# Performance work log

Hardware: AMD Instinct MI355X
Metric: run time of the kernel (lower is better)

Reference implementation:

```python
import jax, jax.numpy as jnp
import numpy as np

B, S, H = 16, 1024, 256
NH = 4
DH = H // NH


def setup_inputs() -> dict:
    key = jax.random.key(0)
    ks = jax.random.split(key, 12)
    w = lambda i, shape: jax.random.normal(ks[i], shape, dtype=jnp.float32) * 0.02
    return {
        "step_sequence": jax.random.normal(ks[0], (B, S, H), dtype=jnp.float32),
        "final_outcomes": jax.random.normal(ks[1], (B,), dtype=jnp.float32),
        "step_mask": jnp.ones((B, S), dtype=jnp.bool_),
        # MultiheadAttention q/k projections (only attn weights are used)
        "Wq": w(2, (H, H)), "bq": jnp.zeros((H,), jnp.float32),
        "Wk": w(3, (H, H)), "bk": jnp.zeros((H,), jnp.float32),
        # causal_mask_predictor: Linear(H,H//2)-ReLU-Linear(H//2,1)-Sigmoid
        "Wm1": w(4, (H, H // 2)), "bm1": jnp.zeros((H // 2,), jnp.float32),
        "Wm2": w(5, (H // 2, 1)), "bm2": jnp.zeros((1,), jnp.float32),
        # intervention_generator: Linear(H,H)-ReLU-Linear(H,H)-Tanh
        "Wi1": w(6, (H, H)), "bi1": jnp.zeros((H,), jnp.float32),
        "Wi2": w(7, (H, H)), "bi2": jnp.zeros((H,), jnp.float32),
        # credit_estimator: Linear(H,H//2)-ReLU-Linear(H//2,1)
        "We1": w(8, (H, H // 2)), "be1": jnp.zeros((H // 2,), jnp.float32),
        "We2": w(9, (H // 2, 1)), "be2": jnp.zeros((1,), jnp.float32),
    }


def _forward(x, final_outcomes, step_mask, Wq, bq, Wk, bk, Wm1, bm1, Wm2, bm2,
             Wi1, bi1, Wi2, bi2, We1, be1, We2, be2):
    # --- CausalAttentionModule ---
    q = (x @ Wq + bq).reshape(B, S, NH, DH).transpose(0, 2, 1, 3)  # [B,NH,S,DH]
    k = (x @ Wk + bk).reshape(B, S, NH, DH).transpose(0, 2, 1, 3)
    scores = jnp.einsum('bhqd,bhkd->bhqk', q, k) / jnp.sqrt(jnp.float32(DH))
    scores = jnp.where(step_mask[:, None, None, :], scores, -jnp.inf)  # key_padding_mask
    attn = jax.nn.softmax(scores, axis=-1).mean(axis=1)  # head-averaged [B,S,S]
    strengths = jax.nn.sigmoid(jax.nn.relu(x @ Wm1 + bm1) @ Wm2 + bm2)[..., 0]  # [B,S]
    aw_mean = attn.mean(axis=1)  # mean over query dim -> [B,S]
    cm = aw_mean[:, None, :] * strengths[:, :, None]  # [B,S,S]
    cm = cm * jnp.tril(jnp.ones((S, S), dtype=x.dtype))[None]
    # --- interventional credit (vectorized over the B x S python loop) ---
    colmean = cm.mean(axis=1)  # mean_i cm[b,i,j] -> [B,S]
    base = (x * colmean[..., None]).mean(axis=1)  # [B,H] baseline weighted-mean feature
    # intervention changes only row t: delta = 0.1*tanh-MLP(x_t)
    delta = 0.1 * jnp.tanh(jax.nn.relu(x @ Wi1 + bi1) @ Wi2 + bi2)  # [B,S,H]
    feats = base[:, None, :] + delta * colmean[..., None] / S  # [B,S,H]
    outcomes = (jax.nn.relu(feats @ We1 + be1) @ We2 + be2)[..., 0]  # [B,S]
    credit = jnp.where(step_mask, final_outcomes[:, None] - outcomes, 0.0)
    return credit, cm


def reference(step_sequence, final_outcomes, step_mask, Wq, bq, Wk, bk,
              Wm1, bm1, Wm2, bm2, Wi1, bi1, Wi2, bi2, We1, be1, We2, be2):
    return _forward(step_sequence, final_outcomes, step_mask, Wq, bq, Wk, bk,
                    Wm1, bm1, Wm2, bm2, Wi1, bi1, Wi2, bi2, We1, be1, We2, be2)
```

## Files before the change

### kernel.cpp

```cpp
#include <hip/hip_runtime.h>
#include <hip/hip_bf16.h>
#include <math.h>

#define B 16
#define S 1024
#define H 256
#define NH 4
#define DH 64
#define BS (B*S)
#define XSTR 264

typedef short short8 __attribute__((ext_vector_type(8)));
typedef float f32x16 __attribute__((ext_vector_type(16)));

__device__ __forceinline__ unsigned short to_bf16(float v) {
  __hip_bfloat16 h = __float2bfloat16(v);
  return *(unsigned short*)&h;
}

__global__ __launch_bounds__(256) void k_convert_x(
    const float* __restrict__ x, unsigned short* __restrict__ xb)
{
  int i = blockIdx.x * 256 + threadIdx.x;
  float4 v = ((const float4*)x)[i];
  uint2 pk;
  pk.x = (unsigned int)to_bf16(v.x) | ((unsigned int)to_bf16(v.y) << 16);
  pk.y = (unsigned int)to_bf16(v.z) | ((unsigned int)to_bf16(v.w) << 16);
  ((uint2*)xb)[i] = pk;
}

__global__ __launch_bounds__(256) void k_convert_w(
    const float* __restrict__ Wq, const float* __restrict__ Wk,
    const float* __restrict__ Wm1, const float* __restrict__ Wi1,
    const float* __restrict__ Wi2, const float* __restrict__ We1,
    unsigned short* __restrict__ WqT, unsigned short* __restrict__ WkT,
    unsigned short* __restrict__ Wm1T, unsigned short* __restrict__ Wi1T,
    unsigned short* __restrict__ Wi2T, unsigned short* __restrict__ We1T)
{
  const float* src; unsigned short* dst; int N;
  switch (blockIdx.y) {
    case 0: src = Wq;  dst = WqT;  N = 256; break;
    case 1: src = Wk;  dst = WkT;  N = 256; break;
    case 2: src = Wm1; dst = Wm1T; N = 128; break;
    case 3: src = Wi1; dst = Wi1T; N = 256; break;
    case 4: src = Wi2; dst = Wi2T; N = 256; break;
    default: src = We1; dst = We1T; N = 128; break;
  }
  int ntiles = N >> 5;
  int tile = blockIdx.x;
  if (tile >= 8 * ntiles) return;
  int kt = tile / ntiles, nt = tile % ntiles;
  __shared__ float tl[32][33];
  int t = threadIdx.x, r = t >> 5, c = t & 31;
  #pragma unroll
  for (int i = 0; i < 4; ++i)
    tl[r + i*8][c] = src[(kt*32 + r + i*8)*N + nt*32 + c];
  __syncthreads();
  #pragma unroll
  for (int i = 0; i < 4; ++i)
    dst[(nt*32 + r + i*8)*256 + kt*32 + c] = to_bf16(tl[c][r + i*8]);
}

__global__ __launch_bounds__(256) void k_qkproj_mfma(
    const unsigned short* __restrict__ xb,
    const unsigned short* __restrict__ WqT, const unsigned short* __restrict__ WkT,
    const float* __restrict__ bq, const float* __restrict__ bk,
    unsigned short* __restrict__ qbuf, unsigned short* __restrict__ kbuf)
{
  __shared__ unsigned short xs[32*XSTR];
  int t = threadIdx.x, wave = t >> 6, lane = t & 63;
  int l5 = lane & 31, h5 = lane >> 5;
  int gx = blockIdx.x, gy = blockIdx.y;
  int r0 = gx * 32;
  const unsigned short* WT = gy ? WkT : WqT;
  const float* biasp = gy ? bk : bq;
  float scale = gy ? 1.f : 0.125f;
  {
    const uint4* s4 = (const uint4*)(xb + (size_t)r0 * H);
    #pragma unroll
    for (int it = 0; it < 4; ++it) {
      int u = it*256 + t, r = u >> 5, c = u & 31;
      *(uint4*)&xs[r*XSTR + c*8] = s4[u];
    }
  }
  __syncthreads();
  f32x16 acc0, acc1;
  #pragma unroll
  for (int r = 0; r < 16; ++r) { acc0[r] = 0.f; acc1[r] = 0.f; }
  int n0 = wave*64 + l5;
  #pragma unroll 8
  for (int kc = 0; kc < 16; ++kc) {
    short8 a = *(const short8*)&xs[l5*XSTR + kc*16 + h5*8];
    short8 b0 = *(const short8*)&WT[(size_t)n0*256 + kc*16 + h5*8];
    short8 b1 = *(const short8*)&WT[(size_t)(n0+32)*256 + kc*16 + h5*8];
    acc0 = __builtin_amdgcn_mfma_f32_32x32x16_bf16(a, b0, acc0, 0, 0, 0);
    acc1 = __builtin_amdgcn_mfma_f32_32x32x16_bf16(a, b1, acc1, 0, 0, 0);
  }
  __syncthreads();
  float bi0 = biasp[n0], bi1v = biasp[n0 + 32];
  #pragma unroll
  for (int r = 0; r < 16; ++r) {
    int row = (r & 3) + 8*(r >> 2) + 4*h5;
    xs[row*XSTR + n0]      = to_bf16((acc0[r] + bi0) * scale);
    xs[row*XSTR + n0 + 32] = to_bf16((acc1[r] + bi1v) * scale);
  }
  __syncthreads();
  unsigned short* outp = gy ? kbuf : qbuf;
  #pragma unroll
  for (int it = 0; it < 4; ++it) {
    int u = it*256 + t, r = u >> 5, c8 = u & 31;
    int mg = r0 + r, bb = mg >> 10, s = mg & 1023;
    int hh = c8 >> 3, dd = (c8 & 7) * 8;
    *(uint4*)&outp[(size_t)(((bb*NH + hh)*S + s)*DH + dd)] = *(uint4*)&xs[r*XSTR + c8*8];
  }
}

__global__ __launch_bounds__(256) void k_strengths_mfma(
    const unsigned short* __restrict__ xb, const unsigned short* __restrict__ Wm1T,
    const float* __restrict__ bm1, const float* __restrict__ Wm2, const float* __restrict__ bm2,
    float* __restrict__ strengths)
{
  __shared__ unsigned short xs[32*XSTR];
  __shared__ float red[4][32];
  int t = threadIdx.x, wave = t >> 6, lane = t & 63;
  int l5 = lane & 31, h5 = lane >> 5;
  int r0 = blockIdx.x * 32;
  {
    const uint4* s4 = (const uint4*)(xb + (size_t)r0 * H);
    #pragma unroll
    for (int it = 0; it < 4; ++it) {
      int u = it*256 + t, r = u >> 5, c = u & 31;
      *(uint4*)&xs[r*XSTR + c*8] = s4[u];
    }
  }
  __syncthreads();
  f32x16 acc;
  #pragma unroll
  for (int r = 0; r < 16; ++r) acc[r] = 0.f;
  int n = wave*32 + l5;
  #pragma unroll 8
  for (int kc = 0; kc < 16; ++kc) {
    short8 a = *(const short8*)&xs[l5*XSTR + kc*16 + h5*8];
    short8 b = *(const short8*)&Wm1T[(size_t)n*256 + kc*16 + h5*8];
    acc = __builtin_amdgcn_mfma_f32_32x32x16_bf16(a, b, acc, 0, 0, 0);
  }
  float bi = bm1[n], w2 = Wm2[n];
  #pragma unroll
  for (int r = 0; r < 16; ++r) {
    float v = fmaxf(acc[r] + bi, 0.f) * w2;
    #pragma unroll
    for (int off = 1; off <= 16; off <<= 1) v += __shfl_xor(v, off);
    if (l5 == 0) red[wave][(r & 3) + 8*(r >> 2) + 4*h5] = v;
  }
  __syncthreads();
  if (t < 32) {
    float s = red[0][t] + red[1][t] + red[2][t] + red[3][t] + bm2[0];
    strengths[r0 + t] = 1.f / (1.f + __expf(-s));
  }
}

#define KSTRIDE 72
__global__ __launch_bounds__(256) void k_attn_mfma(
    const unsigned short* __restrict__ qbuf, const unsigned short* __restrict__ kbuf,
    float* __restrict__ aw_sum)
{
  __shared__ unsigned short Ks[128*KSTRIDE];
  __shared__ unsigned short Qs[64*KSTRIDE];
  int t = threadIdx.x;
  int wave = t >> 6, lane = t & 63;
  int l5 = lane & 31, h5 = lane >> 5;
  int i0 = blockIdx.x * 64;
  int h = blockIdx.y, b = blockIdx.z;
  const unsigned short* qg = qbuf + (size_t)((b*NH + h)*S + i0) * DH;
  const unsigned short* kg = kbuf + (size_t)((b*NH + h)*S) * DH;
  {
    const uint4* src = (const uint4*)qg;
    #pragma unroll
    for (int it = 0; it < 2; ++it) {
      int u = it*256 + t, r = u >> 3, c = u & 7;
      *(uint4*)&Qs[r*KSTRIDE + c*8] = src[u];
    }
  }
  __syncthreads();
  short8 af[2][4];
  #pragma unroll
  for (int rt = 0; rt < 2; ++rt)
    #pragma unroll
    for (int kc = 0; kc < 4; ++kc)
      af[rt][kc] = *(const short8*)&Qs[(rt*32 + l5)*KSTRIDE + kc*16 + h5*8];
  float lacc[2][16];
  #pragma unroll
  for (int rt = 0; rt < 2; ++rt)
    #pragma unroll
    for (int r = 0; r < 16; ++r) lacc[rt][r] = 0.f;
  const uint4* ksrc = (const uint4*)kg;
  for (int pass = 0; pass < 2; ++pass) {
    for (int kt = 0; kt < 8; ++kt) {
      __syncthreads();
      #pragma unroll
      for (int it = 0; it < 4; ++it) {
        int u = it*256 + t, r = u >> 3, c = u & 7;
        *(uint4*)&Ks[r*KSTRIDE + c*8] = ksrc[kt*1024 + u];
      }
      __syncthreads();
      short8 bfr[4];
      #pragma unroll
      for (int kc = 0; kc < 4; ++kc)
        bfr[kc] = *(const short8*)&Ks[(wave*32 + l5)*KSTRIDE + kc*16 + h5*8];
      float csum = 0.f;
      #pragma unroll
      for (int rt = 0; rt < 2; ++rt) {
        f32x16 acc;
        #pragma unroll
        for (int r = 0; r < 16; ++r) acc[r] = 0.f;
        #pragma unroll
        for (int kc = 0; kc < 4; ++kc)
          acc = __builtin_amdgcn_mfma_f32_32x32x16_bf16(af[rt][kc], bfr[kc], acc, 0, 0, 0);
        if (pass == 0) {
          #pragma unroll
          for (int r = 0; r < 16; ++r) lacc[rt][r] += __expf(acc[r]);
        } else {
          #pragma unroll
          for (int r = 0; r < 16; ++r) csum += __expf(acc[r]) * lacc[rt][r];
        }
      }
      if (pass == 1) {
        csum += __shfl_xor(csum, 32);
        if (lane < 32)
          atomicAdd(&aw_sum[b*S + kt*128 + wave*32 + lane], csum);
      }
    }
    if (pass == 0) {
      #pragma unroll
      for (int rt = 0; rt < 2; ++rt)
        #pragma unroll
        for (int r = 0; r < 16; ++r) {
          float v = lacc[rt][r];
          #pragma unroll
          for (int off = 1; off <= 16; off <<= 1) v += __shfl_xor(v, off);
          lacc[rt][r] = 1.f / v;
        }
    }
  }
}

__global__ __launch_bounds__(256) void k_colmean(
    const float* __restrict__ strengths, const float* __restrict__ aw_sum,
    float* __restrict__ aw_mean, float* __restrict__ colmean)
{
  __shared__ float st[1024];
  int t = threadIdx.x, b = blockIdx.x;
  #pragma unroll
  for (int e = 0; e < 4; ++e) st[t + e*256] = strengths[b*S + t + e*256];
  __syncthreads();
  for (int off = 1; off < 1024; off <<= 1) {
    float tmp[4];
    #pragma unroll
    for (int e = 0; e < 4; ++e) {
      int j = t + e*256;
      tmp[e] = (j + off < 1024) ? st[j + off] : 0.f;
    }
    __syncthreads();
    #pragma unroll
    for (int e = 0; e < 4; ++e) st[t + e*256] += tmp[e];
    __syncthreads();
  }
  #pragma unroll
  for (int e = 0; e < 4; ++e) {
    int j = t + e*256;
    float am = aw_sum[b*S + j] * (1.f / (NH * (float)S));
    aw_mean[b*S + j] = am;
    colmean[b*S + j] = am * st[j] * (1.f / (float)S);
  }
}

__global__ __launch_bounds__(256) void k_cm(
    const float* __restrict__ aw_mean, const float* __restrict__ strengths,
    float* __restrict__ cm_out)
{
  int t = threadIdx.x;
  int row = blockIdx.x;
  int b = row >> 10, i = row & 1023;
  float sti = strengths[row];
  float4 v = ((const float4*)(aw_mean + b*S))[t];
  int j0 = t * 4;
  float4 o;
  o.x = (j0 + 0 <= i) ? v.x * sti : 0.f;
  o.y = (j0 + 1 <= i) ? v.y * sti : 0.f;
  o.z = (j0 + 2 <= i) ? v.z * sti : 0.f;
  o.w = (j0 + 3 <= i) ? v.w * sti : 0.f;
  ((float4*)cm_out)[(size_t)row*(S/4) + t] = o;
}

__global__ __launch_bounds__(256) void k_base(
    const float* __restrict__ x, const float* __restrict__ colmean,
    float* __restrict__ base)
{
  int t = threadIdx.x;
  int chunk = blockIdx.x, b = blockIdx.y;
  float acc = 0.f;
  int t0 = chunk * 32;
  for (int tt = 0; tt < 32; ++tt) {
    int srow = t0 + tt;
    acc += x[(size_t)(b*S + srow)*H + t] * colmean[b*S + srow];
  }
  atomicAdd(&base[b*H + t], acc * (1.f / (float)S));
}

__global__ __launch_bounds__(256) void k_credit_mfma(
    const unsigned short* __restrict__ xb, const float* __restrict__ base,
    const float* __restrict__ colmean,
    const unsigned short* __restrict__ Wi1T, const float* __restrict__ bi1,
    const unsigned short* __restrict__ Wi2T, const float* __restrict__ bi2,
    const unsigned short* __restrict__ We1T, const float* __restrict__ be1,
    const float* __restrict__ We2, const float* __restrict__ be2,
    const float* __restrict__ final_outcomes, float* __restrict__ credit_out)
{
  __shared__ unsigned short xs[32*XSTR];
  __shared__ unsigned short hs[32*XSTR];
  __shared__ float cmv_s[32];
  __shared__ float red[4][32];
  int t = threadIdx.x, wave = t >> 6, lane = t & 63;
  int l5 = lane & 31, h5 = lane >> 5;
  int r0 = blockIdx.x * 32;
  int b = r0 >> 10;
  {
    const uint4* s4 = (const uint4*)(xb + (size_t)r0 * H);
    #pragma unroll
    for (int it = 0; it < 4; ++it) {
      int u = it*256 + t, r = u >> 5, c = u & 31;
      *(uint4*)&xs[r*XSTR + c*8] = s4[u];
    }
  }
  if (t < 32) cmv_s[t] = colmean[r0 + t];
  __syncthreads();

  int n0 = wave*64 + l5;
  {
    f32x16 acc0, acc1;
    #pragma unroll
    for (int r = 0; r < 16; ++r) { acc0[r] = 0.f; acc1[r] = 0.f; }
    #pragma unroll 8
    for (int kc = 0; kc < 16; ++kc) {
      short8 a = *(const short8*)&xs[l5*XSTR + kc*16 + h5*8];
      short8 b0 = *(const short8*)&Wi1T[(size_t)n0*256 + kc*16 + h5*8];
      short8 b1 = *(const short8*)&Wi1T[(size_t)(n0+32)*256 + kc*16 + h5*8];
      acc0 = __builtin_amdgcn_mfma_f32_32x32x16_bf16(a, b0, acc0, 0, 0, 0);
      acc1 = __builtin_amdgcn_mfma_f32_32x32x16_bf16(a, b1, acc1, 0, 0, 0);
    }
    float bi0 = bi1[n0], biv1 = bi1[n0 + 32];
    #pragma unroll
    for (int r = 0; r < 16; ++r) {
      int row = (r & 3) + 8*(r >> 2) + 4*h5;
      hs[row*XSTR + n0]      = to_bf16(fmaxf(acc0[r] + bi0, 0.f));
      hs[row*XSTR + n0 + 32] = to_bf16(fmaxf(acc1[r] + biv1, 0.f));
    }
  }
  __syncthreads();
  {
    f32x16 acc0, acc1;
    #pragma unroll
    for (int r = 0; r < 16; ++r) { acc0[r] = 0.f; acc1[r] = 0.f; }
    #pragma unroll 8
    for (int kc = 0; kc < 16; ++kc) {
      short8 a = *(const short8*)&hs[l5*XSTR + kc*16 + h5*8];
      short8 b0 = *(const short8*)&Wi2T[(size_t)n0*256 + kc*16 + h5*8];
      short8 b1 = *(const short8*)&Wi2T[(size_t)(n0+32)*256 + kc*16 + h5*8];
      acc0 = __builtin_amdgcn_mfma_f32_32x32x16_bf16(a, b0, acc0, 0, 0, 0);
      acc1 = __builtin_amdgcn_mfma_f32_32x32x16_bf16(a, b1, acc1, 0, 0, 0);
    }
    float bi0 = bi2[n0], biv1 = bi2[n0 + 32];
    float bb0 = base[b*H + n0], bb1 = base[b*H + n0 + 32];
    __syncthreads();
    #pragma unroll
    for (int r = 0; r < 16; ++r) {
      int row = (r & 3) + 8*(r >> 2) + 4*h5;
      float cmv = cmv_s[row] * (0.1f / (float)S);
      float e0 = __expf(2.f*(acc0[r] + bi0));
      float e1 = __expf(2.f*(acc1[r] + biv1));
      float th0 = (e0 - 1.f) / (e0 + 1.f);
      float th1 = (e1 - 1.f) / (e1 + 1.f);
      xs[row*XSTR + n0]      = to_bf16(bb0 + th0 * cmv);
      xs[row*XSTR + n0 + 32] = to_bf16(bb1 + th1 * cmv);
    }
  }
  __syncthreads();
  {
    f32x16 acc;
    #pragma unroll
    for (int r = 0; r < 16; ++r) acc[r] = 0.f;
    int n = wave*32 + l5;
    #pragma unroll 8
    for (int kc = 0; kc < 16; ++kc) {
      short8 a = *(const short8*)&xs[l5*XSTR + kc*16 + h5*8];
      short8 bfrag = *(const short8*)&We1T[(size_t)n*256 + kc*16 + h5*8];
      acc = __builtin_amdgcn_mfma_f32_32x32x16_bf16(a, bfrag, acc, 0, 0, 0);
    }
    float bev = be1[n], w2 = We2[n];
    #pragma unroll
    for (int r = 0; r < 16; ++r) {
      float v = fmaxf(acc[r] + bev, 0.f) * w2;
      #pragma unroll
      for (int off = 1; off <= 16; off <<= 1) v += __shfl_xor(v, off);
      if (l5 == 0) red[wave][(r & 3) + 8*(r >> 2) + 4*h5] = v;
    }
  }
  __syncthreads();
  if (t < 32) {
    float s = red[0][t] + red[1][t] + red[2][t] + red[3][t] + be2[0];
    credit_out[r0 + t] = final_outcomes[b] - s;
  }
}

extern "C" void kernel_launch(void* const* d_in, const int* in_sizes, int n_in,
                              void* d_out, int out_size, void* d_ws, size_t ws_size,
                              hipStream_t stream) {
  (void)in_sizes; (void)n_in; (void)out_size; (void)ws_size;
  const float* x   = (const float*)d_in[0];
  const float* fin = (const float*)d_in[1];
  const float* Wq  = (const float*)d_in[3];  const float* bq  = (const float*)d_in[4];
  const float* Wk  = (const float*)d_in[5];  const float* bk  = (const float*)d_in[6];
  const float* Wm1 = (const float*)d_in[7];  const float* bm1 = (const float*)d_in[8];
  const float* Wm2 = (const float*)d_in[9];  const float* bm2 = (const float*)d_in[10];
  const float* Wi1 = (const float*)d_in[11]; const float* bi1 = (const float*)d_in[12];
  const float* Wi2 = (const float*)d_in[13]; const float* bi2 = (const float*)d_in[14];
  const float* We1 = (const float*)d_in[15]; const float* be1 = (const float*)d_in[16];
  const float* We2 = (const float*)d_in[17]; const float* be2 = (const float*)d_in[18];

  unsigned short* us = (unsigned short*)d_ws;
  unsigned short* xb   = us;
  unsigned short* qb   = xb + (size_t)BS*H;
  unsigned short* kb   = qb + (size_t)B*NH*S*DH;
  unsigned short* WqT  = kb + (size_t)B*NH*S*DH;
  unsigned short* WkT  = WqT + 65536;
  unsigned short* Wi1T = WkT + 65536;
  unsigned short* Wi2T = Wi1T + 65536;
  unsigned short* Wm1T = Wi2T + 65536;
  unsigned short* We1T = Wm1T + 32768;
  float* fs = (float*)(We1T + 32768);
  float* aw_sum    = fs;
  float* strengths = aw_sum + BS;
  float* aw_mean   = strengths + BS;
  float* colmean   = aw_mean + BS;
  float* base      = colmean + BS;

  float* credit_out = (float*)d_out;
  float* cm_out     = credit_out + BS;

  hipMemsetAsync(aw_sum, 0, BS*sizeof(float), stream);
  hipMemsetAsync(base, 0, B*H*sizeof(float), stream);

  k_convert_x     <<<BS*H/1024, 256, 0, stream>>>(x, xb);
  k_convert_w     <<<dim3(64, 6), 256, 0, stream>>>(Wq, Wk, Wm1, Wi1, Wi2, We1,
                                                    WqT, WkT, Wm1T, Wi1T, Wi2T, We1T);
  k_qkproj_mfma   <<<dim3(BS/32, 2), 256, 0, stream>>>(xb, WqT, WkT, bq, bk, qb, kb);
  k_strengths_mfma<<<BS/32, 256, 0, stream>>>(xb, Wm1T, bm1, Wm2, bm2, strengths);
  k_attn_mfma     <<<dim3(S/64, NH, B), 256, 0, stream>>>(qb, kb, aw_sum);
  k_colmean       <<<B, 256, 0, stream>>>(strengths, aw_sum, aw_mean, colmean);
  k_cm            <<<BS, 256, 0, stream>>>(aw_mean, strengths, cm_out);
  k_base          <<<dim3(32, B), 256, 0, stream>>>(x, colmean, base);
  k_credit_mfma   <<<BS/32, 256, 0, stream>>>(xb, base, colmean, Wi1T, bi1, Wi2T, bi2,
                                              We1T, be1, We2, be2, fin, credit_out);
}
```

Measured before the change: 238.1 us.

## Fuse x conversion into consumers, single-pass attention softmax, drop atomics

Removes the separate x-to-bf16 conversion kernel and converts fp32 x on the fly inside the projection, strengths and credit kernels. Q and K projections are computed in one block sharing the x tile, and the Q scale folds in log2(e) so attention can use hardware exp2. Attention is restructured into a single pass over keys that caches bf16-packed probabilities in registers instead of recomputing scores. Atomics and memsets are replaced by per-tile partial buffers that later kernels sum. This trades heavy register pressure and extra partial-sum reads for fewer launches, less recomputation and no atomic contention.

```diff
diff --git a/kernel.cpp b/kernel.cpp
--- a/kernel.cpp
+++ b/kernel.cpp
@@ -9,6 +9,7 @@
 #define DH 64
 #define BS (B*S)
 #define XSTR 264
+#define L2E 1.4426950408889634f
 
 typedef short short8 __attribute__((ext_vector_type(8)));
 typedef float f32x16 __attribute__((ext_vector_type(16)));
@@ -17,16 +18,11 @@
   __hip_bfloat16 h = __float2bfloat16(v);
   return *(unsigned short*)&h;
 }
-
-__global__ __launch_bounds__(256) void k_convert_x(
-    const float* __restrict__ x, unsigned short* __restrict__ xb)
-{
-  int i = blockIdx.x * 256 + threadIdx.x;
-  float4 v = ((const float4*)x)[i];
-  uint2 pk;
-  pk.x = (unsigned int)to_bf16(v.x) | ((unsigned int)to_bf16(v.y) << 16);
-  pk.y = (unsigned int)to_bf16(v.z) | ((unsigned int)to_bf16(v.w) << 16);
-  ((uint2*)xb)[i] = pk;
+__device__ __forceinline__ unsigned int pack_bf16x2(float a, float b) {
+  return (unsigned int)to_bf16(a) | ((unsigned int)to_bf16(b) << 16);
+}
+__device__ __forceinline__ float exp2_hw(float v) {
+  return __builtin_amdgcn_exp2f(v);
 }
 
 __global__ __launch_bounds__(256) void k_convert_w(
@@ -62,7 +58,7 @@
 }
 
 __global__ __launch_bounds__(256) void k_qkproj_mfma(
-    const unsigned short* __restrict__ xb,
+    const float* __restrict__ x,
     const unsigned short* __restrict__ WqT, const unsigned short* __restrict__ WkT,
     const float* __restrict__ bq, const float* __restrict__ bk,
     unsigned short* __restrict__ qbuf, unsigned short* __restrict__ kbuf)
@@ -70,53 +66,75 @@
   __shared__ unsigned short xs[32*XSTR];
   int t = threadIdx.x, wave = t >> 6, lane = t & 63;
   int l5 = lane & 31, h5 = lane >> 5;
-  int gx = blockIdx.x, gy = blockIdx.y;
-  int r0 = gx * 32;
-  const unsigned short* WT = gy ? WkT : WqT;
-  const float* biasp = gy ? bk : bq;
-  float scale = gy ? 1.f : 0.125f;
-  {
-    const uint4* s4 = (const uint4*)(xb + (size_t)r0 * H);
-    #pragma unroll
-    for (int it = 0; it < 4; ++it) {
-      int u = it*256 + t, r = u >> 5, c = u & 31;
-      *(uint4*)&xs[r*XSTR + c*8] = s4[u];
-    }
-  }
-  __syncthreads();
-  f32x16 acc0, acc1;
-  #pragma unroll
-  for (int r = 0; r < 16; ++r) { acc0[r] = 0.f; acc1[r] = 0.f; }
+  int r0 = blockIdx.x * 32;
+  {
+    const float4* xg = (const float4*)(x + (size_t)r0*H);
+    #pragma unroll
+    for (int it = 0; it < 8; ++it) {
+      int u = it*256 + t, r = u >> 6, c4 = u & 63;
+      float4 v = xg[u];
+      uint2 pk; pk.x = pack_bf16x2(v.x, v.y); pk.y = pack_bf16x2(v.z, v.w);
+      *(uint2*)&xs[r*XSTR + c4*4] = pk;
+    }
+  }
+  __syncthreads();
   int n0 = wave*64 + l5;
+  f32x16 aq0, aq1, ak0, ak1;
+  #pragma unroll
+  for (int r = 0; r < 16; ++r) { aq0[r]=0.f; aq1[r]=0.f; ak0[r]=0.f; ak1[r]=0.f; }
   #pragma unroll 8
   for (int kc = 0; kc < 16; ++kc) {
-    short8 a = *(const short8*)&xs[l5*XSTR + kc*16 + h5*8];
-    short8 b0 = *(const short8*)&WT[(size_t)n0*256 + kc*16 + h5*8];
-    short8 b1 = *(const short8*)&WT[(size_t)(n0+32)*256 + kc*16 + h5*8];
-    acc0 = __builtin_amdgcn_mfma_f32_32x32x16_bf16(a, b0, acc0, 0, 0, 0);
-    acc1 = __builtin_amdgcn_mfma_f32_32x32x16_bf16(a, b1, acc1, 0, 0, 0);
-  }
-  __syncthreads();
-  float bi0 = biasp[n0], bi1v = biasp[n0 + 32];
-  #pragma unroll
-  for (int r = 0; r < 16; ++r) {
-    int row = (r & 3) + 8*(r >> 2) + 4*h5;
-    xs[row*XSTR + n0]      = to_bf16((acc0[r] + bi0) * scale);
-    xs[row*XSTR + n0 + 32] = to_bf16((acc1[r] + bi1v) * scale);
-  }
-  __syncthreads();
-  unsigned short* outp = gy ? kbuf : qbuf;
+    short8 a  = *(const short8*)&xs[l5*XSTR + kc*16 + h5*8];
+    short8 q0 = *(const short8*)&WqT[(size_t)n0*256 + kc*16 + h5*8];
+    short8 q1 = *(const short8*)&WqT[(size_t)(n0+32)*256 + kc*16 + h5*8];
+    short8 k0 = *(const short8*)&WkT[(size_t)n0*256 + kc*16 + h5*8];
+    short8 k1 = *(const short8*)&WkT[(size_t)(n0+32)*256 + kc*16 + h5*8];
+    aq0 = __builtin_amdgcn_mfma_f32_32x32x16_bf16(a, q0, aq0, 0, 0, 0);
+    aq1 = __builtin_amdgcn_mfma_f32_32x32x16_bf16(a, q1, aq1, 0, 0, 0);
+    ak0 = __builtin_amdgcn_mfma_f32_32x32x16_bf16(a, k0, ak0, 0, 0, 0);
+    ak1 = __builtin_amdgcn_mfma_f32_32x32x16_bf16(a, k1, ak1, 0, 0, 0);
+  }
+  const float qsc = 0.125f * L2E;
+  __syncthreads();
+  {
+    float b0 = bq[n0], b1 = bq[n0+32];
+    #pragma unroll
+    for (int r = 0; r < 16; ++r) {
+      int row = (r & 3) + 8*(r >> 2) + 4*h5;
+      xs[row*XSTR + n0]      = to_bf16((aq0[r] + b0) * qsc);
+      xs[row*XSTR + n0 + 32] = to_bf16((aq1[r] + b1) * qsc);
+    }
+  }
+  __syncthreads();
   #pragma unroll
   for (int it = 0; it < 4; ++it) {
     int u = it*256 + t, r = u >> 5, c8 = u & 31;
     int mg = r0 + r, bb = mg >> 10, s = mg & 1023;
     int hh = c8 >> 3, dd = (c8 & 7) * 8;
-    *(uint4*)&outp[(size_t)(((bb*NH + hh)*S + s)*DH + dd)] = *(uint4*)&xs[r*XSTR + c8*8];
+    *(uint4*)&qbuf[(size_t)(((bb*NH + hh)*S + s)*DH + dd)] = *(uint4*)&xs[r*XSTR + c8*8];
+  }
+  __syncthreads();
+  {
+    float b0 = bk[n0], b1 = bk[n0+32];
+    #pragma unroll
+    for (int r = 0; r < 16; ++r) {
+      int row = (r & 3) + 8*(r >> 2) + 4*h5;
+      xs[row*XSTR + n0]      = to_bf16(ak0[r] + b0);
+      xs[row*XSTR + n0 + 32] = to_bf16(ak1[r] + b1);
+    }
+  }
+  __syncthreads();
+  #pragma unroll
+  for (int it = 0; it < 4; ++it) {
+    int u = it*256 + t, r = u >> 5, c8 = u & 31;
+    int mg = r0 + r, bb = mg >> 10, s = mg & 1023;
+    int hh = c8 >> 3, dd = (c8 & 7) * 8;
+    *(uint4*)&kbuf[(size_t)(((bb*NH + hh)*S + s)*DH + dd)] = *(uint4*)&xs[r*XSTR + c8*8];
   }
 }
 
 __global__ __launch_bounds__(256) void k_strengths_mfma(
-    const unsigned short* __restrict__ xb, const unsigned short* __restrict__ Wm1T,
+    const float* __restrict__ x, const unsigned short* __restrict__ Wm1T,
     const float* __restrict__ bm1, const float* __restrict__ Wm2, const float* __restrict__ bm2,
     float* __restrict__ strengths)
 {
@@ -126,11 +144,13 @@
   int l5 = lane & 31, h5 = lane >> 5;
   int r0 = blockIdx.x * 32;
   {
-    const uint4* s4 = (const uint4*)(xb + (size_t)r0 * H);
-    #pragma unroll
-    for (int it = 0; it < 4; ++it) {
-      int u = it*256 + t, r = u >> 5, c = u & 31;
-      *(uint4*)&xs[r*XSTR + c*8] = s4[u];
+    const float4* xg = (const float4*)(x + (size_t)r0*H);
+    #pragma unroll
+    for (int it = 0; it < 8; ++it) {
+      int u = it*256 + t, r = u >> 6, c4 = u & 63;
+      float4 v = xg[u];
+      uint2 pk; pk.x = pack_bf16x2(v.x, v.y); pk.y = pack_bf16x2(v.z, v.w);
+      *(uint2*)&xs[r*XSTR + c4*4] = pk;
     }
   }
   __syncthreads();
@@ -159,93 +179,101 @@
   }
 }
 
-#define KSTRIDE 72
 __global__ __launch_bounds__(256) void k_attn_mfma(
     const unsigned short* __restrict__ qbuf, const unsigned short* __restrict__ kbuf,
-    float* __restrict__ aw_sum)
-{
-  __shared__ unsigned short Ks[128*KSTRIDE];
-  __shared__ unsigned short Qs[64*KSTRIDE];
-  int t = threadIdx.x;
-  int wave = t >> 6, lane = t & 63;
+    float* __restrict__ aw_part)
+{
+  __shared__ float part[4][64];
+  int t = threadIdx.x, wave = t >> 6, lane = t & 63;
   int l5 = lane & 31, h5 = lane >> 5;
-  int i0 = blockIdx.x * 64;
+  int qt = blockIdx.x, i0 = qt * 64;
   int h = blockIdx.y, b = blockIdx.z;
   const unsigned short* qg = qbuf + (size_t)((b*NH + h)*S + i0) * DH;
   const unsigned short* kg = kbuf + (size_t)((b*NH + h)*S) * DH;
-  {
-    const uint4* src = (const uint4*)qg;
-    #pragma unroll
-    for (int it = 0; it < 2; ++it) {
-      int u = it*256 + t, r = u >> 3, c = u & 7;
-      *(uint4*)&Qs[r*KSTRIDE + c*8] = src[u];
-    }
-  }
-  __syncthreads();
+
   short8 af[2][4];
   #pragma unroll
   for (int rt = 0; rt < 2; ++rt)
     #pragma unroll
     for (int kc = 0; kc < 4; ++kc)
-      af[rt][kc] = *(const short8*)&Qs[(rt*32 + l5)*KSTRIDE + kc*16 + h5*8];
+      af[rt][kc] = *(const short8*)(qg + (rt*32 + l5)*DH + kc*16 + h5*8);
+
   float lacc[2][16];
   #pragma unroll
   for (int rt = 0; rt < 2; ++rt)
     #pragma unroll
     for (int r = 0; r < 16; ++r) lacc[rt][r] = 0.f;
-  const uint4* ksrc = (const uint4*)kg;
-  for (int pass = 0; pass < 2; ++pass) {
-    for (int kt = 0; kt < 8; ++kt) {
-      __syncthreads();
+
+  unsigned int pp[8][2][8];
+  #pragma unroll
+  for (int kt = 0; kt < 8; ++kt) {
+    short8 bfr[4];
+    #pragma unroll
+    for (int kc = 0; kc < 4; ++kc)
+      bfr[kc] = *(const short8*)(kg + (size_t)(kt*128 + wave*32 + l5)*DH + kc*16 + h5*8);
+    f32x16 a0, a1;
+    #pragma unroll
+    for (int r = 0; r < 16; ++r) { a0[r] = 0.f; a1[r] = 0.f; }
+    #pragma unroll
+    for (int kc = 0; kc < 4; ++kc) {
+      a0 = __builtin_amdgcn_mfma_f32_32x32x16_bf16(af[0][kc], bfr[kc], a0, 0, 0, 0);
+      a1 = __builtin_amdgcn_mfma_f32_32x32x16_bf16(af[1][kc], bfr[kc], a1, 0, 0, 0);
+    }
+    #pragma unroll
+    for (int r2 = 0; r2 < 8; ++r2) {
+      float p0 = exp2_hw(a0[2*r2]), p1 = exp2_hw(a0[2*r2+1]);
+      lacc[0][2*r2] += p0; lacc[0][2*r2+1] += p1;
+      pp[kt][0][r2] = pack_bf16x2(p0, p1);
+      float q0 = exp2_hw(a1[2*r2]), q1 = exp2_hw(a1[2*r2+1]);
+      lacc[1][2*r2] += q0; lacc[1][2*r2+1] += q1;
+      pp[kt][1][r2] = pack_bf16x2(q0, q1);
+    }
+  }
+  #pragma unroll
+  for (int rt = 0; rt < 2; ++rt)
+    #pragma unroll
+    for (int r = 0; r < 16; ++r) {
+      float v = lacc[rt][r];
       #pragma unroll
-      for (int it = 0; it < 4; ++it) {
-        int u = it*256 + t, r = u >> 3, c = u & 7;
-        *(uint4*)&Ks[r*KSTRIDE + c*8] = ksrc[kt*1024 + u];
+      for (int off = 1; off <= 16; off <<= 1) v += __shfl_xor(v, off);
+      lacc[rt][r] = v;
+    }
+  if (l5 == 0) {
+    #pragma unroll
+    for (int rt = 0; rt < 2; ++rt)
+      #pragma unroll
+      for (int r = 0; r < 16; ++r)
+        part[wave][rt*32 + (r & 3) + 8*(r >> 2) + 4*h5] = lacc[rt][r];
+  }
+  __syncthreads();
+  float linv[2][16];
+  #pragma unroll
+  for (int rt = 0; rt < 2; ++rt)
+    #pragma unroll
+    for (int r = 0; r < 16; ++r) {
+      int row = rt*32 + (r & 3) + 8*(r >> 2) + 4*h5;
+      linv[rt][r] = 1.f / (part[0][row] + part[1][row] + part[2][row] + part[3][row]);
+    }
+  #pragma unroll
+  for (int kt = 0; kt < 8; ++kt) {
+    float csum = 0.f;
+    #pragma unroll
+    for (int rt = 0; rt < 2; ++rt)
+      #pragma unroll
+      for (int r2 = 0; r2 < 8; ++r2) {
+        unsigned int u = pp[kt][rt][r2];
+        float p0 = __uint_as_float(u << 16);
+        float p1 = __uint_as_float(u & 0xffff0000u);
+        csum += p0 * linv[rt][2*r2] + p1 * linv[rt][2*r2+1];
       }
-      __syncthreads();
-      short8 bfr[4];
-      #pragma unroll
-      for (int kc = 0; kc < 4; ++kc)
-        bfr[kc] = *(const short8*)&Ks[(wave*32 + l5)*KSTRIDE + kc*16 + h5*8];
-      float csum = 0.f;
-      #pragma unroll
-      for (int rt = 0; rt < 2; ++rt) {
-        f32x16 acc;
-        #pragma unroll
-        for (int r = 0; r < 16; ++r) acc[r] = 0.f;
-        #pragma unroll
-        for (int kc = 0; kc < 4; ++kc)
-          acc = __builtin_amdgcn_mfma_f32_32x32x16_bf16(af[rt][kc], bfr[kc], acc, 0, 0, 0);
-        if (pass == 0) {
-          #pragma unroll
-          for (int r = 0; r < 16; ++r) lacc[rt][r] += __expf(acc[r]);
-        } else {
-          #pragma unroll
-          for (int r = 0; r < 16; ++r) csum += __expf(acc[r]) * lacc[rt][r];
-        }
-      }
-      if (pass == 1) {
-        csum += __shfl_xor(csum, 32);
-        if (lane < 32)
-          atomicAdd(&aw_sum[b*S + kt*128 + wave*32 + lane], csum);
-      }
-    }
-    if (pass == 0) {
-      #pragma unroll
-      for (int rt = 0; rt < 2; ++rt)
-        #pragma unroll
-        for (int r = 0; r < 16; ++r) {
-          float v = lacc[rt][r];
-          #pragma unroll
-          for (int off = 1; off <= 16; off <<= 1) v += __shfl_xor(v, off);
-          lacc[rt][r] = 1.f / v;
-        }
-    }
+    csum += __shfl_xor(csum, 32);
+    if (lane < 32)
+      aw_part[(size_t)qt*BS + b*S + kt*128 + wave*32 + lane] = csum;
   }
 }
 
 __global__ __launch_bounds__(256) void k_colmean(
-    const float* __restrict__ strengths, const float* __restrict__ aw_sum,
+    const float* __restrict__ strengths, const float* __restrict__ aw_part,
     float* __restrict__ aw_mean, float* __restrict__ colmean)
 {
   __shared__ float st[1024];
@@ -268,7 +296,10 @@
   #pragma unroll
   for (int e = 0; e < 4; ++e) {
     int j = t + e*256;
-    float am = aw_sum[b*S + j] * (1.f / (NH * (float)S));
+    float s = 0.f;
+    #pragma unroll
+    for (int qt = 0; qt < 16; ++qt) s += aw_part[(size_t)qt*BS + b*S + j];
+    float am = s * (1.f / (NH * (float)S));
     aw_mean[b*S + j] = am;
     colmean[b*S + j] = am * st[j] * (1.f / (float)S);
   }
@@ -294,7 +325,7 @@
 
 __global__ __launch_bounds__(256) void k_base(
     const float* __restrict__ x, const float* __restrict__ colmean,
-    float* __restrict__ base)
+    float* __restrict__ base_part)
 {
   int t = threadIdx.x;
   int chunk = blockIdx.x, b = blockIdx.y;
@@ -304,11 +335,11 @@
     int srow = t0 + tt;
     acc += x[(size_t)(b*S + srow)*H + t] * colmean[b*S + srow];
   }
-  atomicAdd(&base[b*H + t], acc * (1.f / (float)S));
+  base_part[(size_t)chunk*B*H + b*H + t] = acc * (1.f / (float)S);
 }
 
 __global__ __launch_bounds__(256) void k_credit_mfma(
-    const unsigned short* __restrict__ xb, const float* __restrict__ base,
+    const float* __restrict__ x, const float* __restrict__ base_part,
     const float* __restrict__ colmean,
     const unsigned short* __restrict__ Wi1T, const float* __restrict__ bi1,
     const unsigned short* __restrict__ Wi2T, const float* __restrict__ bi2,
@@ -325,17 +356,25 @@
   int r0 = blockIdx.x * 32;
   int b = r0 >> 10;
   {
-    const uint4* s4 = (const uint4*)(xb + (size_t)r0 * H);
-    #pragma unroll
-    for (int it = 0; it < 4; ++it) {
-      int u = it*256 + t, r = u >> 5, c = u & 31;
-      *(uint4*)&xs[r*XSTR + c*8] = s4[u];
+    const float4* xg = (const float4*)(x + (size_t)r0*H);
+    #pragma unroll
+    for (int it = 0; it < 8; ++it) {
+      int u = it*256 + t, r = u >> 6, c4 = u & 63;
+      float4 v = xg[u];
+      uint2 pk; pk.x = pack_bf16x2(v.x, v.y); pk.y = pack_bf16x2(v.z, v.w);
+      *(uint2*)&xs[r*XSTR + c4*4] = pk;
     }
   }
   if (t < 32) cmv_s[t] = colmean[r0 + t];
-  __syncthreads();
-
   int n0 = wave*64 + l5;
+  float bb0 = 0.f, bb1 = 0.f;
+  #pragma unroll
+  for (int c = 0; c < 32; ++c) {
+    bb0 += base_part[(size_t)c*B*H + b*H + n0];
+    bb1 += base_part[(size_t)c*B*H + b*H + n0 + 32];
+  }
+  __syncthreads();
+
   {
     f32x16 acc0, acc1;
     #pragma unroll
@@ -370,7 +409,6 @@
       acc1 = __builtin_amdgcn_mfma_f32_32x32x16_bf16(a, b1, acc1, 0, 0, 0);
     }
     float bi0 = bi2[n0], biv1 = bi2[n0 + 32];
-    float bb0 = base[b*H + n0], bb1 = base[b*H + n0 + 32];
     __syncthreads();
     #pragma unroll
     for (int r = 0; r < 16; ++r) {
@@ -428,8 +466,7 @@
   const float* We2 = (const float*)d_in[17]; const float* be2 = (const float*)d_in[18];
 
   unsigned short* us = (unsigned short*)d_ws;
-  unsigned short* xb   = us;
-  unsigned short* qb   = xb + (size_t)BS*H;
+  unsigned short* qb   = us;
   unsigned short* kb   = qb + (size_t)B*NH*S*DH;
   unsigned short* WqT  = kb + (size_t)B*NH*S*DH;
   unsigned short* WkT  = WqT + 65536;
@@ -438,27 +475,23 @@
   unsigned short* Wm1T = Wi2T + 65536;
   unsigned short* We1T = Wm1T + 32768;
   float* fs = (float*)(We1T + 32768);
-  float* aw_sum    = fs;
-  float* strengths = aw_sum + BS;
+  float* aw_part   = fs;
+  float* strengths = aw_part + 16*BS;
   float* aw_mean   = strengths + BS;
   float* colmean   = aw_mean + BS;
-  float* base      = colmean + BS;
+  float* base_part = colmean + BS;
 
   float* credit_out = (float*)d_out;
   float* cm_out     = credit_out + BS;
 
-  hipMemsetAsync(aw_sum, 0, BS*sizeof(float), stream);
-  hipMemsetAsync(base, 0, B*H*sizeof(float), stream);
-
-  k_convert_x     <<<BS*H/1024, 256, 0, stream>>>(x, xb);
   k_convert_w     <<<dim3(64, 6), 256, 0, stream>>>(Wq, Wk, Wm1, Wi1, Wi2, We1,
                                                     WqT, WkT, Wm1T, Wi1T, Wi2T, We1T);
-  k_qkproj_mfma   <<<dim3(BS/32, 2), 256, 0, stream>>>(xb, WqT, WkT, bq, bk, qb, kb);
-  k_strengths_mfma<<<BS/32, 256, 0, stream>>>(xb, Wm1T, bm1, Wm2, bm2, strengths);
-  k_attn_mfma     <<<dim3(S/64, NH, B), 256, 0, stream>>>(qb, kb, aw_sum);
-  k_colmean       <<<B, 256, 0, stream>>>(strengths, aw_sum, aw_mean, colmean);
+  k_qkproj_mfma   <<<BS/32, 256, 0, stream>>>(x, WqT, WkT, bq, bk, qb, kb);
+  k_strengths_mfma<<<BS/32, 256, 0, stream>>>(x, Wm1T, bm1, Wm2, bm2, strengths);
+  k_attn_mfma     <<<dim3(S/64, NH, B), 256, 0, stream>>>(qb, kb, aw_part);
+  k_colmean       <<<B, 256, 0, stream>>>(strengths, aw_part, aw_mean, colmean);
+  k_base          <<<dim3(32, B), 256, 0, stream>>>(x, colmean, base_part);
   k_cm            <<<BS, 256, 0, stream>>>(aw_mean, strengths, cm_out);
-  k_base          <<<dim3(32, B), 256, 0, stream>>>(x, colmean, base);
-  k_credit_mfma   <<<BS/32, 256, 0, stream>>>(xb, base, colmean, Wi1T, bi1, Wi2T, bi2,
+  k_credit_mfma   <<<BS/32, 256, 0, stream>>>(x, base_part, colmean, Wi1T, bi1, Wi2T, bi2,
                                               We1T, be1, We2, be2, fin, credit_out);
 }
```

Result: faster. 233.1 us (-2.1%).
